# Kernel tuning notes

Hardware: AMD Instinct MI355X
Metric: run time of the kernel (lower is better)

The kernel has to match this reference:

```python
import jax, jax.numpy as jnp
import numpy as np

D_MODEL = 1024
H = 16
D_K = D_MODEL // H


def setup_inputs() -> dict:
    key = jax.random.key(0)
    ks = jax.random.split(key, 10)
    B, S = 2, 2048
    s = 1.0 / np.sqrt(D_MODEL)
    x = jax.random.normal(ks[0], (B, S, D_MODEL), dtype=jnp.float32)
    mask = jax.random.randint(ks[1], (B, 1, S, S), 0, 2, dtype=jnp.int32)
    w_q = jax.random.normal(ks[2], (D_MODEL, D_MODEL), dtype=jnp.float32) * s
    b_q = jnp.zeros((D_MODEL,), dtype=jnp.float32)
    w_k = jax.random.normal(ks[3], (D_MODEL, D_MODEL), dtype=jnp.float32) * s
    b_k = jnp.zeros((D_MODEL,), dtype=jnp.float32)
    w_v = jax.random.normal(ks[4], (D_MODEL, D_MODEL), dtype=jnp.float32) * s
    b_v = jnp.zeros((D_MODEL,), dtype=jnp.float32)
    w_o = jax.random.normal(ks[5], (D_MODEL, D_MODEL), dtype=jnp.float32) * s
    b_o = jnp.zeros((D_MODEL,), dtype=jnp.float32)
    return {"x": x, "mask": mask, "w_q": w_q, "b_q": b_q, "w_k": w_k,
            "b_k": b_k, "w_v": w_v, "b_v": b_v, "w_o": w_o, "b_o": b_o}


def reference(x, mask, w_q, b_q, w_k, b_k, w_v, b_v, w_o, b_o):
    B, S, _ = x.shape
    # projections; weights stored as (in, out) equivalents of torch Linear
    q = (x @ w_q + b_q).reshape(B, S, H, D_K).transpose(0, 2, 1, 3)  # bhsd
    k = (x @ w_k + b_k).reshape(B, S, H, D_K).transpose(0, 2, 1, 3)
    v = (x @ w_v + b_v).reshape(B, S, H, D_K).transpose(0, 2, 1, 3)
    scores = jnp.einsum('bhqd,bhkd->bhqk', q, k) / jnp.sqrt(jnp.float32(D_K))
    scores = jnp.where(mask == 0, jnp.float32(-1e9), scores)
    attn = jax.nn.softmax(scores, axis=-1)  # dropout omitted (eval mode)
    out = jnp.einsum('bhqk,bhkd->bhqd', attn, v)
    out = out.transpose(0, 2, 1, 3).reshape(B, S, D_MODEL)
    return out @ w_o + b_o
```

## Files before the change

### kernel.cpp

```cpp
#include <hip/hip_runtime.h>
#include <hip/hip_bf16.h>
#include <stdint.h>

#define D_MODEL 1024
#define NH 16
#define DK 64
#define SEQ 2048
#define BATCH 2
#define NTOK (BATCH * SEQ)

typedef __bf16 bf16;
typedef float f32x4 __attribute__((ext_vector_type(4)));
typedef __bf16 bf16x8 __attribute__((ext_vector_type(8)));
typedef __bf16 bf16x4 __attribute__((ext_vector_type(4)));

#define QSCALE 0.18033687932432668f

__device__ __forceinline__ void gload_lds16(const void* g, void* l) {
  __builtin_amdgcn_global_load_lds(
      (const __attribute__((address_space(1))) void*)g,
      (__attribute__((address_space(3))) void*)l, 16, 0, 0);
}


__global__ void cast_x_kernel(const float* __restrict__ x, bf16* __restrict__ xb) {
  int i = blockIdx.x * 256 + threadIdx.x;
  float4 v = reinterpret_cast<const float4*>(x)[i];
  bf16x4 o;
  o[0] = (bf16)v.x; o[1] = (bf16)v.y; o[2] = (bf16)v.z; o[3] = (bf16)v.w;
  reinterpret_cast<bf16x4*>(xb)[i] = o;
}

__global__ void transpose_w_kernel(const float* __restrict__ wq, const float* __restrict__ wk,
                                   const float* __restrict__ wv, const float* __restrict__ wo,
                                   bf16* __restrict__ wt) {
  __shared__ float tile[32][33];
  const int jt = blockIdx.x;
  const int kt = blockIdx.y;
  const int tx = threadIdx.x & 31, ty = threadIdx.x >> 5;
  const int j0 = jt * 32;
  const int sel = j0 >> 10;
  const float* w = (sel == 0) ? wq : (sel == 1) ? wk : (sel == 2) ? wv : wo;
  const int jj0 = j0 & 1023;
#pragma unroll
  for (int i = 0; i < 4; ++i)
    tile[ty + i * 8][tx] = w[(size_t)(kt * 32 + ty + i * 8) * 1024 + jj0 + tx];
  __syncthreads();
#pragma unroll
  for (int i = 0; i < 4; ++i)
    wt[(size_t)(j0 + ty + i * 8) * 1024 + kt * 32 + tx] = (bf16)tile[tx][ty + i * 8];
}

__global__ void pack_mask_kernel(const int* __restrict__ mask, unsigned long long* __restrict__ bits) {
  int gt = blockIdx.x * 256 + threadIdx.x;
  int wid = gt >> 6;
  int l = gt & 63;
  int m = mask[(size_t)wid * 64 + l];
  unsigned long long b = __ballot(m != 0);
  if (l == 0) bits[wid] = b;
}

__global__ __launch_bounds__(256) void gemm_qkv(
    const bf16* __restrict__ A, const bf16* __restrict__ Bt,
    const float* __restrict__ b0, const float* __restrict__ b1, const float* __restrict__ b2,
    bf16* __restrict__ out_q, bf16* __restrict__ out_k, bf16* __restrict__ out_vt) {
  __shared__ __align__(16) bf16 As[128 * 32];
  __shared__ __align__(16) bf16 Bs[128 * 32];
  const int tid = threadIdx.x;
  const int w = tid >> 6, l = tid & 63;
  const int wr = w >> 1, wc = w & 1;
  const int m0 = blockIdx.y * 128, n0 = blockIdx.x * 128;
  f32x4 acc[4][4] = {};
  const int lrow = l >> 2;
  const int lc8 = (l & 3) * 8;
  char* AsB = (char*)As;
  char* BsB = (char*)Bs;

  for (int k0 = 0; k0 < 1024; k0 += 32) {
#pragma unroll
    for (int is = 0; is < 2; ++is) {
      int arow = m0 + is * 64 + w * 16 + lrow;
      gload_lds16(A + (size_t)arow * 1024 + k0 + lc8, AsB + is * 4096 + w * 1024);
      int brow = n0 + is * 64 + w * 16 + lrow;
      gload_lds16(Bt + (size_t)brow * 1024 + k0 + lc8, BsB + is * 4096 + w * 1024);
    }
    __syncthreads();
    bf16x8 af[4], bfr[4];
#pragma unroll
    for (int m = 0; m < 4; ++m)
      af[m] = *reinterpret_cast<const bf16x8*>(As + (wr * 64 + m * 16 + (l & 15)) * 32 + (l >> 4) * 8);
#pragma unroll
    for (int n = 0; n < 4; ++n)
      bfr[n] = *reinterpret_cast<const bf16x8*>(Bs + (wc * 64 + n * 16 + (l & 15)) * 32 + (l >> 4) * 8);
#pragma unroll
    for (int m = 0; m < 4; ++m)
#pragma unroll
      for (int n = 0; n < 4; ++n)
        acc[m][n] = __builtin_amdgcn_mfma_f32_16x16x32_bf16(af[m], bfr[n], acc[m][n], 0, 0, 0);
    __syncthreads();
  }

#pragma unroll
  for (int m = 0; m < 4; ++m) {
    int ib = m0 + wr * 64 + m * 16 + 4 * (l >> 4);
#pragma unroll
    for (int n = 0; n < 4; ++n) {
      int j = n0 + wc * 64 + n * 16 + (l & 15);
      int sel = j >> 10, jj = j & 1023;
      const float* bp = (sel == 0) ? b0 : (sel == 1) ? b1 : b2;
      float bias = bp[jj];
      if (sel == 0) {
#pragma unroll
        for (int r = 0; r < 4; ++r)
          out_q[(size_t)(ib + r) * 1024 + jj] = (bf16)((acc[m][n][r] + bias) * QSCALE);
      } else if (sel == 1) {
#pragma unroll
        for (int r = 0; r < 4; ++r)
          out_k[(size_t)(ib + r) * 1024 + jj] = (bf16)(acc[m][n][r] + bias);
      } else {
        int hh = jj >> 6, dd = jj & 63;
        int bb = ib >> 11, ss = ib & 2047;
        bf16x4 v;
#pragma unroll
        for (int r = 0; r < 4; ++r) v[r] = (bf16)(acc[m][n][r] + bias);
        *reinterpret_cast<bf16x4*>(out_vt + ((size_t)(bb * NH + hh) * DK + dd) * SEQ + ss) = v;
      }
    }
  }
}

__global__ __launch_bounds__(256) void gemm_out(
    const bf16* __restrict__ A, const bf16* __restrict__ Bt,
    const float* __restrict__ bias, float* __restrict__ out) {
  __shared__ __align__(16) bf16 As[64 * 32];
  __shared__ __align__(16) bf16 Bs[64 * 32];
  const int tid = threadIdx.x;
  const int w = tid >> 6, l = tid & 63;
  const int wr = w >> 1, wc = w & 1;
  const int m0 = blockIdx.y * 64, n0 = blockIdx.x * 64;
  f32x4 acc[2][2] = {};
  const int srow = w * 16 + (l >> 2);
  const int sc8 = (l & 3) * 8;

  for (int k0 = 0; k0 < 1024; k0 += 32) {
    gload_lds16(A + (size_t)(m0 + srow) * 1024 + k0 + sc8, (char*)As + w * 1024);
    gload_lds16(Bt + (size_t)(n0 + srow) * 1024 + k0 + sc8, (char*)Bs + w * 1024);
    __syncthreads();
    bf16x8 af[2], bfr[2];
#pragma unroll
    for (int m = 0; m < 2; ++m)
      af[m] = *reinterpret_cast<const bf16x8*>(As + (wr * 32 + m * 16 + (l & 15)) * 32 + (l >> 4) * 8);
#pragma unroll
    for (int n = 0; n < 2; ++n)
      bfr[n] = *reinterpret_cast<const bf16x8*>(Bs + (wc * 32 + n * 16 + (l & 15)) * 32 + (l >> 4) * 8);
#pragma unroll
    for (int m = 0; m < 2; ++m)
#pragma unroll
      for (int n = 0; n < 2; ++n)
        acc[m][n] = __builtin_amdgcn_mfma_f32_16x16x32_bf16(af[m], bfr[n], acc[m][n], 0, 0, 0);
    __syncthreads();
  }

#pragma unroll
  for (int m = 0; m < 2; ++m) {
    int ib = m0 + wr * 32 + m * 16 + 4 * (l >> 4);
#pragma unroll
    for (int n = 0; n < 2; ++n) {
      int j = n0 + wc * 32 + n * 16 + (l & 15);
      float bv = bias[j];
#pragma unroll
      for (int r = 0; r < 4; ++r)
        out[(size_t)(ib + r) * 1024 + j] = acc[m][n][r] + bv;
    }
  }
}

__global__ __launch_bounds__(256, 4) void attn_kernel(
    const bf16* __restrict__ qb, const bf16* __restrict__ kb,
    const bf16* __restrict__ vt, const unsigned long long* __restrict__ mbits,
    bf16* __restrict__ ob) {
  __shared__ __align__(16) bf16 Ks[64 * 64];
  __shared__ __align__(16) bf16 Vs[64 * 64];
  __shared__ __align__(16) bf16 Ps[4][16 * 64];
  const int tid = threadIdx.x;
  const int w = tid >> 6, l = tid & 63;
  const int qt = blockIdx.x, h = blockIdx.y, b = blockIdx.z;
  const int q0 = qt * 64;
  const int qrow = q0 + w * 16;
  const int tok0 = b * SEQ + qrow;

  bf16x8 qf[2];
#pragma unroll
  for (int kk = 0; kk < 2; ++kk)
    qf[kk] = *reinterpret_cast<const bf16x8*>(
        qb + (size_t)(tok0 + (l & 15)) * 1024 + h * 64 + kk * 32 + (l >> 4) * 8);

  float lsum[4] = {0.f, 0.f, 0.f, 0.f};
  f32x4 oacc[4] = {};

  const int swz = ((l & 7) ^ (l >> 3)) * 8;
  const bf16* ksrc = kb + (size_t)(b * SEQ) * 1024 + h * 64;
  const bf16* vsrc = vt + (size_t)(b * NH + h) * DK * SEQ;
  const unsigned long long* mrow = mbits + ((size_t)(b * SEQ + qrow + 4 * (l >> 4)) << 5);
  char* KsB = (char*)Ks;
  char* VsB = (char*)Vs;

  for (int kt = 0; kt < 32; ++kt) {
    unsigned long long mw[4];
#pragma unroll
    for (int r = 0; r < 4; ++r) mw[r] = mrow[(size_t)(r << 5) + kt];

#pragma unroll
    for (int i = 0; i < 2; ++i) {
      int row = i * 32 + w * 8 + (l >> 3);
      gload_lds16(ksrc + (size_t)(kt * 64 + row) * 1024 + swz, KsB + i * 4096 + w * 1024);
      gload_lds16(vsrc + (size_t)row * SEQ + kt * 64 + swz, VsB + i * 4096 + w * 1024);
    }
    __syncthreads();

    f32x4 sa[4] = {};
#pragma unroll
    for (int kk = 0; kk < 2; ++kk) {
      bf16x8 kf[4];
      int c = kk * 4 + (l >> 4);
#pragma unroll
      for (int n = 0; n < 4; ++n) {
        int rr = n * 16 + (l & 15);
        kf[n] = *reinterpret_cast<const bf16x8*>(Ks + rr * 64 + ((c ^ (rr & 7)) << 3));
      }
#pragma unroll
      for (int n = 0; n < 4; ++n)
        sa[n] = __builtin_amdgcn_mfma_f32_16x16x32_bf16(qf[kk], kf[n], sa[n], 0, 0, 0);
    }

#pragma unroll
    for (int r = 0; r < 4; ++r) {
      int prow = 4 * (l >> 4) + r;
      unsigned long long sh = mw[r] >> (l & 15);
      unsigned int blo = (unsigned int)sh, bhi = (unsigned int)(sh >> 32);
      float p0 = (blo & 1u) ? __builtin_amdgcn_exp2f(sa[0][r]) : 0.f;
      float p1 = (blo & 0x10000u) ? __builtin_amdgcn_exp2f(sa[1][r]) : 0.f;
      float p2 = (bhi & 1u) ? __builtin_amdgcn_exp2f(sa[2][r]) : 0.f;
      float p3 = (bhi & 0x10000u) ? __builtin_amdgcn_exp2f(sa[3][r]) : 0.f;
      lsum[r] += (p0 + p1) + (p2 + p3);
      int colb = l & 7;
      int swzr = (prow & 7);
#pragma unroll
      for (int n = 0; n < 4; ++n) {
        int col = n * 16 + (l & 15);
        float p = (n == 0) ? p0 : (n == 1) ? p1 : (n == 2) ? p2 : p3;
        Ps[w][prow * 64 + (((col >> 3) ^ swzr) << 3) + colb] = (bf16)p;
      }
    }

#pragma unroll
    for (int kk = 0; kk < 2; ++kk) {
      int c = kk * 4 + (l >> 4);
      bf16x8 pa, vf[4];
      {
        int rr = l & 15;
        pa = *reinterpret_cast<const bf16x8*>(Ps[w] + rr * 64 + ((c ^ (rr & 7)) << 3));
      }
#pragma unroll
      for (int dn = 0; dn < 4; ++dn) {
        int rr = dn * 16 + (l & 15);
        vf[dn] = *reinterpret_cast<const bf16x8*>(Vs + rr * 64 + ((c ^ (rr & 7)) << 3));
      }
#pragma unroll
      for (int dn = 0; dn < 4; ++dn)
        oacc[dn] = __builtin_amdgcn_mfma_f32_16x16x32_bf16(pa, vf[dn], oacc[dn], 0, 0, 0);
    }
    __syncthreads();
  }

#pragma unroll
  for (int r = 0; r < 4; ++r) {
    float s = lsum[r];
    s += __shfl_xor(s, 1);
    s += __shfl_xor(s, 2);
    s += __shfl_xor(s, 4);
    s += __shfl_xor(s, 8);
    float inv = 1.f / s;
    int tok = tok0 + 4 * (l >> 4) + r;
#pragma unroll
    for (int dn = 0; dn < 4; ++dn)
      ob[(size_t)tok * 1024 + h * 64 + dn * 16 + (l & 15)] = (bf16)(oacc[dn][r] * inv);
  }
}

extern "C" void kernel_launch(void* const* d_in, const int* in_sizes, int n_in,
                              void* d_out, int out_size, void* d_ws, size_t ws_size,
                              hipStream_t stream) {
  const float* x = (const float*)d_in[0];
  const int* mask = (const int*)d_in[1];
  const float* wq = (const float*)d_in[2];
  const float* bq = (const float*)d_in[3];
  const float* wk = (const float*)d_in[4];
  const float* bk = (const float*)d_in[5];
  const float* wv = (const float*)d_in[6];
  const float* bv = (const float*)d_in[7];
  const float* wo = (const float*)d_in[8];
  const float* bo = (const float*)d_in[9];
  float* out = (float*)d_out;

  char* ws = (char*)d_ws;
  bf16* xb = (bf16*)(ws + (size_t)0);
  bf16* wt = (bf16*)(ws + ((size_t)8 << 20));
  bf16* qb = (bf16*)(ws + ((size_t)16 << 20));
  bf16* kb = (bf16*)(ws + ((size_t)24 << 20));
  bf16* vtb = (bf16*)(ws + ((size_t)32 << 20));
  bf16* ob = (bf16*)(ws + ((size_t)40 << 20));
  unsigned long long* mbits = (unsigned long long*)(ws + ((size_t)48 << 20));

  cast_x_kernel<<<4096, 256, 0, stream>>>(x, xb);
  transpose_w_kernel<<<dim3(128, 32), 256, 0, stream>>>(wq, wk, wv, wo, wt);
  pack_mask_kernel<<<32768, 256, 0, stream>>>(mask, mbits);
  gemm_qkv<<<dim3(24, 32), 256, 0, stream>>>(xb, wt, bq, bk, bv, qb, kb, vtb);
  attn_kernel<<<dim3(32, NH, BATCH), 256, 0, stream>>>(qb, kb, vtb, mbits, ob);
  gemm_out<<<dim3(16, 64), 256, 0, stream>>>(ob, wt + (size_t)3072 * 1024, bo, out);
}
```

Before: 255.3 us.

## Fuse prep kernels, double-buffer attention K/V loads, enlarge output GEMM tile

Merges the x cast, weight transpose and mask packing into one kernel launch to cut launch overhead. The attention kernel now double-buffers K/V tiles in LDS and prefetches the next tile while computing the current one, using explicit vmcnt waits and barriers. The output GEMM tile grows from 64x64 to 128x64 so each block does more work per B load. The hand-written vmcnt counts make correctness depend on the exact number of outstanding loads, and the extra LDS may lower attention occupancy.

```diff
diff --git a/kernel.cpp b/kernel.cpp
--- a/kernel.cpp
+++ b/kernel.cpp
@@ -22,42 +22,44 @@
       (__attribute__((address_space(3))) void*)l, 16, 0, 0);
 }
 
-
-__global__ void cast_x_kernel(const float* __restrict__ x, bf16* __restrict__ xb) {
-  int i = blockIdx.x * 256 + threadIdx.x;
-  float4 v = reinterpret_cast<const float4*>(x)[i];
-  bf16x4 o;
-  o[0] = (bf16)v.x; o[1] = (bf16)v.y; o[2] = (bf16)v.z; o[3] = (bf16)v.w;
-  reinterpret_cast<bf16x4*>(xb)[i] = o;
-}
-
-__global__ void transpose_w_kernel(const float* __restrict__ wq, const float* __restrict__ wk,
-                                   const float* __restrict__ wv, const float* __restrict__ wo,
-                                   bf16* __restrict__ wt) {
+__global__ void prep_kernel(const float* __restrict__ x, bf16* __restrict__ xb,
+                            const float* __restrict__ wq, const float* __restrict__ wk,
+                            const float* __restrict__ wv, const float* __restrict__ wo,
+                            bf16* __restrict__ wt,
+                            const int* __restrict__ mask, unsigned long long* __restrict__ bits) {
   __shared__ float tile[32][33];
-  const int jt = blockIdx.x;
-  const int kt = blockIdx.y;
-  const int tx = threadIdx.x & 31, ty = threadIdx.x >> 5;
-  const int j0 = jt * 32;
-  const int sel = j0 >> 10;
-  const float* w = (sel == 0) ? wq : (sel == 1) ? wk : (sel == 2) ? wv : wo;
-  const int jj0 = j0 & 1023;
-#pragma unroll
-  for (int i = 0; i < 4; ++i)
-    tile[ty + i * 8][tx] = w[(size_t)(kt * 32 + ty + i * 8) * 1024 + jj0 + tx];
-  __syncthreads();
-#pragma unroll
-  for (int i = 0; i < 4; ++i)
-    wt[(size_t)(j0 + ty + i * 8) * 1024 + kt * 32 + tx] = (bf16)tile[tx][ty + i * 8];
-}
-
-__global__ void pack_mask_kernel(const int* __restrict__ mask, unsigned long long* __restrict__ bits) {
-  int gt = blockIdx.x * 256 + threadIdx.x;
-  int wid = gt >> 6;
-  int l = gt & 63;
-  int m = mask[(size_t)wid * 64 + l];
-  unsigned long long b = __ballot(m != 0);
-  if (l == 0) bits[wid] = b;
+  const int bx = blockIdx.x;
+  const int tid = threadIdx.x;
+  if (bx < 4096) {
+    int i = bx * 256 + tid;
+    float4 v = reinterpret_cast<const float4*>(x)[i];
+    bf16x4 o;
+    o[0] = (bf16)v.x; o[1] = (bf16)v.y; o[2] = (bf16)v.z; o[3] = (bf16)v.w;
+    reinterpret_cast<bf16x4*>(xb)[i] = o;
+  } else if (bx < 8192) {
+    int blk = bx - 4096;
+    const int jt = blk & 127;
+    const int kt = blk >> 7;
+    const int tx = tid & 31, ty = tid >> 5;
+    const int j0 = jt * 32;
+    const int sel = j0 >> 10;
+    const float* w = (sel == 0) ? wq : (sel == 1) ? wk : (sel == 2) ? wv : wo;
+    const int jj0 = j0 & 1023;
+#pragma unroll
+    for (int i = 0; i < 4; ++i)
+      tile[ty + i * 8][tx] = w[(size_t)(kt * 32 + ty + i * 8) * 1024 + jj0 + tx];
+    __syncthreads();
+#pragma unroll
+    for (int i = 0; i < 4; ++i)
+      wt[(size_t)(j0 + ty + i * 8) * 1024 + kt * 32 + tx] = (bf16)tile[tx][ty + i * 8];
+  } else {
+    int gt = (bx - 8192) * 256 + tid;
+    int wid = gt >> 6;
+    int l = gt & 63;
+    int m = mask[(size_t)wid * 64 + l];
+    unsigned long long b = __ballot(m != 0);
+    if (l == 0) bits[wid] = b;
+  }
 }
 
 __global__ __launch_bounds__(256) void gemm_qkv(
@@ -132,29 +134,35 @@
 __global__ __launch_bounds__(256) void gemm_out(
     const bf16* __restrict__ A, const bf16* __restrict__ Bt,
     const float* __restrict__ bias, float* __restrict__ out) {
-  __shared__ __align__(16) bf16 As[64 * 32];
+  __shared__ __align__(16) bf16 As[128 * 32];
   __shared__ __align__(16) bf16 Bs[64 * 32];
   const int tid = threadIdx.x;
   const int w = tid >> 6, l = tid & 63;
   const int wr = w >> 1, wc = w & 1;
-  const int m0 = blockIdx.y * 64, n0 = blockIdx.x * 64;
-  f32x4 acc[2][2] = {};
-  const int srow = w * 16 + (l >> 2);
-  const int sc8 = (l & 3) * 8;
+  const int m0 = blockIdx.y * 128, n0 = blockIdx.x * 64;
+  f32x4 acc[4][2] = {};
+  const int lrow = l >> 2;
+  const int lc8 = (l & 3) * 8;
+  char* AsB = (char*)As;
+  char* BsB = (char*)Bs;
 
   for (int k0 = 0; k0 < 1024; k0 += 32) {
-    gload_lds16(A + (size_t)(m0 + srow) * 1024 + k0 + sc8, (char*)As + w * 1024);
-    gload_lds16(Bt + (size_t)(n0 + srow) * 1024 + k0 + sc8, (char*)Bs + w * 1024);
-    __syncthreads();
-    bf16x8 af[2], bfr[2];
-#pragma unroll
-    for (int m = 0; m < 2; ++m)
-      af[m] = *reinterpret_cast<const bf16x8*>(As + (wr * 32 + m * 16 + (l & 15)) * 32 + (l >> 4) * 8);
+#pragma unroll
+    for (int is = 0; is < 2; ++is) {
+      int arow = m0 + is * 64 + w * 16 + lrow;
+      gload_lds16(A + (size_t)arow * 1024 + k0 + lc8, AsB + is * 4096 + w * 1024);
+    }
+    gload_lds16(Bt + (size_t)(n0 + w * 16 + lrow) * 1024 + k0 + lc8, BsB + w * 1024);
+    __syncthreads();
+    bf16x8 af[4], bfr[2];
+#pragma unroll
+    for (int m = 0; m < 4; ++m)
+      af[m] = *reinterpret_cast<const bf16x8*>(As + (wr * 64 + m * 16 + (l & 15)) * 32 + (l >> 4) * 8);
 #pragma unroll
     for (int n = 0; n < 2; ++n)
       bfr[n] = *reinterpret_cast<const bf16x8*>(Bs + (wc * 32 + n * 16 + (l & 15)) * 32 + (l >> 4) * 8);
 #pragma unroll
-    for (int m = 0; m < 2; ++m)
+    for (int m = 0; m < 4; ++m)
 #pragma unroll
       for (int n = 0; n < 2; ++n)
         acc[m][n] = __builtin_amdgcn_mfma_f32_16x16x32_bf16(af[m], bfr[n], acc[m][n], 0, 0, 0);
@@ -162,8 +170,8 @@
   }
 
 #pragma unroll
-  for (int m = 0; m < 2; ++m) {
-    int ib = m0 + wr * 32 + m * 16 + 4 * (l >> 4);
+  for (int m = 0; m < 4; ++m) {
+    int ib = m0 + wr * 64 + m * 16 + 4 * (l >> 4);
 #pragma unroll
     for (int n = 0; n < 2; ++n) {
       int j = n0 + wc * 32 + n * 16 + (l & 15);
@@ -179,8 +187,8 @@
     const bf16* __restrict__ qb, const bf16* __restrict__ kb,
     const bf16* __restrict__ vt, const unsigned long long* __restrict__ mbits,
     bf16* __restrict__ ob) {
-  __shared__ __align__(16) bf16 Ks[64 * 64];
-  __shared__ __align__(16) bf16 Vs[64 * 64];
+  __shared__ __align__(16) bf16 Kbuf[2][64 * 64];
+  __shared__ __align__(16) bf16 Vbuf[2][64 * 64];
   __shared__ __align__(16) bf16 Ps[4][16 * 64];
   const int tid = threadIdx.x;
   const int w = tid >> 6, l = tid & 63;
@@ -202,21 +210,38 @@
   const bf16* ksrc = kb + (size_t)(b * SEQ) * 1024 + h * 64;
   const bf16* vsrc = vt + (size_t)(b * NH + h) * DK * SEQ;
   const unsigned long long* mrow = mbits + ((size_t)(b * SEQ + qrow + 4 * (l >> 4)) << 5);
-  char* KsB = (char*)Ks;
-  char* VsB = (char*)Vs;
-
-  for (int kt = 0; kt < 32; ++kt) {
-    unsigned long long mw[4];
-#pragma unroll
-    for (int r = 0; r < 4; ++r) mw[r] = mrow[(size_t)(r << 5) + kt];
-
+
+  auto STAGE = [&](int buf, int kt) {
+    char* KsB = (char*)Kbuf[buf];
+    char* VsB = (char*)Vbuf[buf];
 #pragma unroll
     for (int i = 0; i < 2; ++i) {
       int row = i * 32 + w * 8 + (l >> 3);
       gload_lds16(ksrc + (size_t)(kt * 64 + row) * 1024 + swz, KsB + i * 4096 + w * 1024);
       gload_lds16(vsrc + (size_t)row * SEQ + kt * 64 + swz, VsB + i * 4096 + w * 1024);
     }
-    __syncthreads();
+  };
+
+  STAGE(0, 0);
+  for (int kt = 0; kt < 32; ++kt) {
+    const int cur = kt & 1;
+    unsigned long long mw[4];
+#pragma unroll
+    for (int r = 0; r < 4; ++r) mw[r] = mrow[(size_t)(r << 5) + kt];
+    __builtin_amdgcn_sched_barrier(0);
+    if (kt < 31) {
+      STAGE(cur ^ 1, kt + 1);
+      __builtin_amdgcn_sched_barrier(0);
+      asm volatile("s_waitcnt vmcnt(8)" ::: "memory");
+    } else {
+      __builtin_amdgcn_sched_barrier(0);
+      asm volatile("s_waitcnt vmcnt(4)" ::: "memory");
+    }
+    __builtin_amdgcn_s_barrier();
+    __builtin_amdgcn_sched_barrier(0);
+
+    const bf16* Ks = Kbuf[cur];
+    const bf16* Vs = Vbuf[cur];
 
     f32x4 sa[4] = {};
 #pragma unroll
@@ -270,7 +295,8 @@
       for (int dn = 0; dn < 4; ++dn)
         oacc[dn] = __builtin_amdgcn_mfma_f32_16x16x32_bf16(pa, vf[dn], oacc[dn], 0, 0, 0);
     }
-    __syncthreads();
+    __builtin_amdgcn_sched_barrier(0);
+    __builtin_amdgcn_s_barrier();
   }
 
 #pragma unroll
@@ -312,10 +338,8 @@
   bf16* ob = (bf16*)(ws + ((size_t)40 << 20));
   unsigned long long* mbits = (unsigned long long*)(ws + ((size_t)48 << 20));
 
-  cast_x_kernel<<<4096, 256, 0, stream>>>(x, xb);
-  transpose_w_kernel<<<dim3(128, 32), 256, 0, stream>>>(wq, wk, wv, wo, wt);
-  pack_mask_kernel<<<32768, 256, 0, stream>>>(mask, mbits);
+  prep_kernel<<<40960, 256, 0, stream>>>(x, xb, wq, wk, wv, wo, wt, mask, mbits);
   gemm_qkv<<<dim3(24, 32), 256, 0, stream>>>(xb, wt, bq, bk, bv, qb, kb, vtb);
   attn_kernel<<<dim3(32, NH, BATCH), 256, 0, stream>>>(qb, kb, vtb, mbits, ob);
-  gemm_out<<<dim3(16, 64), 256, 0, stream>>>(ob, wt + (size_t)3072 * 1024, bo, out);
-}
+  gemm_out<<<dim3(16, 32), 256, 0, stream>>>(ob, wt + (size_t)3072 * 1024, bo, out);
+}
```

Result: faster. 242.0 us (-5.2%).
